# Kernel optimization log

Measured on AMD Instinct MI355X. Metric: run time of the kernel, lower is better.

The kernel has to match this reference:

```python
import jax, jax.numpy as jnp
import numpy as np

N_NODES = 50000
NEG_SLOPE = 0.2

def _segment_softmax(e, seg, n):
    m = jax.ops.segment_max(e, seg, num_segments=n)
    ex = jnp.exp(e - m[seg])
    s = jax.ops.segment_sum(ex, seg, num_segments=n)
    return ex / s[seg]

def _gatv2_layer(x, src, dst, n, Wl, bl, Wr, br, att):
    # GATv2 (heads=1): e_ij = att . leaky_relu(Wl x_j + Wr x_i); msg = alpha * Wl x_j
    xl = x @ Wl + bl            # [N, D] source transform
    xr = x @ Wr + br            # [N, D] target transform
    h = jax.nn.leaky_relu(xl[src] + xr[dst], NEG_SLOPE)  # [E, D]
    e = h @ att                 # [E]
    alpha = _segment_softmax(e, dst, n)
    out = jax.ops.segment_sum(alpha[:, None] * xl[src], dst, num_segments=n)
    return out

def setup_inputs() -> dict:
    key = jax.random.key(0)
    ks = jax.random.split(key, 16)
    N, E, Q, F, D, H = N_NODES, 800000, 200000, 128, 250, 256
    def glorot(k, shape):
        fan = shape[0] + shape[-1]
        return jax.random.uniform(k, shape, jnp.float32, -1.0, 1.0) * np.sqrt(6.0 / fan)
    return {
        "x": jax.random.normal(ks[0], (N, F), jnp.float32),
        "edge_index": jax.random.randint(ks[1], (2, E), 0, N, jnp.int32),
        "query": jax.random.randint(ks[2], (Q, 2), 0, N, jnp.int32),
        "W1l": glorot(ks[3], (F, D)), "b1l": jnp.zeros((D,), jnp.float32),
        "W1r": glorot(ks[4], (F, D)), "b1r": jnp.zeros((D,), jnp.float32),
        "att1": glorot(ks[5], (D,)),
        "W2l": glorot(ks[6], (D, D)), "b2l": jnp.zeros((D,), jnp.float32),
        "W2r": glorot(ks[7], (D, D)), "b2r": jnp.zeros((D,), jnp.float32),
        "att2": glorot(ks[8], (D,)),
        "Wm1": glorot(ks[9], (2 * D, H)), "bm1": jnp.zeros((H,), jnp.float32),
        "Wm2": glorot(ks[10], (H, 1)), "bm2": jnp.zeros((1,), jnp.float32),
    }

def reference(x, edge_index, query, W1l, b1l, W1r, b1r, att1,
              W2l, b2l, W2r, b2r, att2, Wm1, bm1, Wm2, bm2):
    n = x.shape[0]
    # add self loops (PyG default add_self_loops=True)
    loops = jnp.arange(n, dtype=edge_index.dtype)
    src = jnp.concatenate([edge_index[0], loops])
    dst = jnp.concatenate([edge_index[1], loops])
    h = _gatv2_layer(x, src, dst, n, W1l, b1l, W1r, b1r, att1)
    h = jax.nn.relu(h)
    emb = _gatv2_layer(h, src, dst, n, W2l, b2l, W2r, b2r, att2)
    # edge-prediction head: gather pair embeddings, concat, MLP
    pair = jnp.concatenate([emb[query[:, 0]], emb[query[:, 1]]], axis=1)  # [Q, 2D]
    out = jax.nn.relu(pair @ Wm1 + bm1)
    out = jax.nn.relu(out @ Wm2 + bm2)
    return out
```

## Files before the change

kernel.cpp:

```cpp
#include <hip/hip_runtime.h>
#include <hip/hip_fp16.h>
#include <math.h>
#include <stdint.h>

#define NN 50000
#define NE 800000
#define ET (NE + NN)
#define FIN 128
#define DD 250
#define HD 256
#define NQ 200000
#define NEG_SLOPE 0.2f

typedef unsigned short u16;
typedef __attribute__((ext_vector_type(4))) float f32x4;
typedef _Float16 h2v __attribute__((ext_vector_type(2)));
typedef _Float16 f16x8 __attribute__((ext_vector_type(8)));

union H2U { h2v h; unsigned int u; };

__device__ __forceinline__ u16 f2h(float v) {
    __half h = __float2half(v);
    return *reinterpret_cast<u16*>(&h);
}
__device__ __forceinline__ float4 ld4h(const u16* p) {
    uint2 r = *(const uint2*)p;
    __half2 a = *(__half2*)&r.x;
    __half2 b = *(__half2*)&r.y;
    float2 fa = __half22float2(a), fb = __half22float2(b);
    return make_float4(fa.x, fa.y, fb.x, fb.y);
}
__device__ __forceinline__ h2v hmax2v(h2v a, h2v b) {
    return __builtin_elementwise_max(a, b);
}


#define DPPMOV(v, ctrl, rm) \
    ((unsigned int)__builtin_amdgcn_update_dpp(0, (int)(v), (ctrl), (rm), 0xF, true))

__device__ __forceinline__ unsigned int h2_wave_sum63(h2v x) {
    H2U u, t; u.h = x;
    t.u = DPPMOV(u.u, 0x111, 0xF); u.h = u.h + t.h;
    t.u = DPPMOV(u.u, 0x112, 0xF); u.h = u.h + t.h;
    t.u = DPPMOV(u.u, 0x114, 0xF); u.h = u.h + t.h;
    t.u = DPPMOV(u.u, 0x118, 0xF); u.h = u.h + t.h;
    t.u = DPPMOV(u.u, 0x142, 0xA); u.h = u.h + t.h;
    t.u = DPPMOV(u.u, 0x143, 0xC); u.h = u.h + t.h;
    return (unsigned int)__builtin_amdgcn_readlane((int)u.u, 63);
}

__device__ __forceinline__ float f32_wave_sum63(float x) {
    union FU { float f; unsigned int u; } a, t, o;
    a.f = x;
    t.u = DPPMOV(a.u, 0x111, 0xF); a.f += t.f;
    t.u = DPPMOV(a.u, 0x112, 0xF); a.f += t.f;
    t.u = DPPMOV(a.u, 0x114, 0xF); a.f += t.f;
    t.u = DPPMOV(a.u, 0x118, 0xF); a.f += t.f;
    t.u = DPPMOV(a.u, 0x142, 0xA); a.f += t.f;
    t.u = DPPMOV(a.u, 0x143, 0xC); a.f += t.f;
    o.u = (unsigned int)__builtin_amdgcn_readlane((int)a.u, 63);
    return o.f;
}


__global__ __launch_bounds__(256) void scan1_kernel(
    int* __restrict__ cnt, int* __restrict__ rowptr, int* __restrict__ bsum)
{
    __shared__ int buf[256];
    int t = threadIdx.x;
    int i = blockIdx.x * 256 + t;
    int v = (i < NN) ? cnt[i] : 0;
    if (i < NN) cnt[i] = 0;
    buf[t] = v;
    __syncthreads();
#pragma unroll
    for (int off = 1; off < 256; off <<= 1) {
        int add = (t >= off) ? buf[t - off] : 0;
        __syncthreads();
        buf[t] += add;
        __syncthreads();
    }
    if (i < NN) rowptr[i] = buf[t] - v;
    if (t == 255) bsum[blockIdx.x] = buf[255];
}

__global__ __launch_bounds__(256) void scan2_kernel(
    int* __restrict__ bsum, int* __restrict__ rowptr, int nb)
{
    __shared__ int buf[256];
    int t = threadIdx.x;
    int v = (t < nb) ? bsum[t] : 0;
    buf[t] = v;
    __syncthreads();
#pragma unroll
    for (int off = 1; off < 256; off <<= 1) {
        int add = (t >= off) ? buf[t - off] : 0;
        __syncthreads();
        buf[t] += add;
        __syncthreads();
    }
    if (t < nb) bsum[t] = buf[t] - v;
    if (t == 255) rowptr[NN] = buf[255];
}

__global__ __launch_bounds__(256) void scan3_kernel(
    int* __restrict__ rowptr, const int* __restrict__ bsum)
{
    int i = blockIdx.x * 256 + threadIdx.x;
    if (i < NN) rowptr[i] += bsum[blockIdx.x];
}

__global__ void scatter_kernel(const int* __restrict__ ei,
                               const int* __restrict__ rowptr,
                               int* __restrict__ fill,
                               int* __restrict__ ssrc) {
    int k = blockIdx.x * 256 + threadIdx.x;
    if (k >= ET) return;
    int s, d;
    if (k < NE) { s = ei[k]; d = ei[NE + k]; }
    else        { s = k - NE; d = k - NE; }
    int pos = rowptr[d] + atomicAdd(&fill[d], 1);
    ssrc[pos] = s << 9;
}


#define CONVX_BLOCKS 3125

__global__ __launch_bounds__(256) void conv_all(
    const float* __restrict__ x, const int* __restrict__ ei,
    u16* __restrict__ Asp,
    const float* __restrict__ W1l, const float* __restrict__ W1r,
    const float* __restrict__ W2l, const float* __restrict__ W2r,
    const float* __restrict__ Wm1,
    const float* __restrict__ att1, const float* __restrict__ att2,
    u16* __restrict__ W1lT, u16* __restrict__ W1rT,
    u16* __restrict__ W2lT, u16* __restrict__ W2rT,
    u16* __restrict__ WmtT, u16* __restrict__ WmbT,
    u16* __restrict__ atth1, u16* __restrict__ atth2,
    int* __restrict__ cnt)
{
    if (blockIdx.x < CONVX_BLOCKS) {
        int tid = blockIdx.x * 256 + threadIdx.x;
        size_t idx = (size_t)tid * 8;
        if (idx >= (size_t)NN * FIN) return;
        float4 v0 = *(const float4*)(x + idx);
        float4 v1 = *(const float4*)(x + idx + 4);
        ushort4 o0, o1;
        o0.x = f2h(v0.x); o0.y = f2h(v0.y); o0.z = f2h(v0.z); o0.w = f2h(v0.w);
        o1.x = f2h(v1.x); o1.y = f2h(v1.y); o1.z = f2h(v1.z); o1.w = f2h(v1.w);
        *(ushort4*)(Asp + idx) = o0;
        *(ushort4*)(Asp + idx + 4) = o1;
        return;
    }
    int b = blockIdx.x - CONVX_BLOCKS;
    if (b < 1280) {
        const float* W; int K, N, koff, kshift, b0; u16* ot;
        if (b < 128)       { W = W1l; K = FIN; N = DD; koff = 0;  kshift = 7; b0 = 0;    ot = W1lT; }
        else if (b < 256)  { W = W1r; K = FIN; N = DD; koff = 0;  kshift = 7; b0 = 128;  ot = W1rT; }
        else if (b < 512)  { W = W2l; K = DD;  N = DD; koff = 0;  kshift = 8; b0 = 256;  ot = W2lT; }
        else if (b < 768)  { W = W2r; K = DD;  N = DD; koff = 0;  kshift = 8; b0 = 512;  ot = W2rT; }
        else if (b < 1024) { W = Wm1; K = DD;  N = HD; koff = 0;  kshift = 8; b0 = 768;  ot = WmtT; }
        else               { W = Wm1; K = DD;  N = HD; koff = DD; kshift = 8; b0 = 1024; ot = WmbT; }
        int id = (b - b0) * 256 + threadIdx.x;
        int Kp = 1 << kshift;
        int n = id >> kshift, k = id & (Kp - 1);
        float v = (n < N && k < K) ? W[(size_t)(k + koff) * N + n] : 0.f;
        ot[id] = f2h(v);
        return;
    }
    if (b < 1282) {
        const float* a = (b == 1280) ? att1 : att2;
        u16* o = (b == 1280) ? atth1 : atth2;
        int id = threadIdx.x;
        o[id] = f2h(id < DD ? a[id] : 0.f);
        return;
    }
    int k = (b - 1282) * 256 + threadIdx.x;
    if (k >= ET) return;
    int d = (k < NE) ? ei[NE + k] : (k - NE);
    atomicAdd(&cnt[d], 1);
}


#define AP 40

__global__ __launch_bounds__(512) void gemm_pair(
    const u16* __restrict__ A, int Kp,
    const u16* __restrict__ B0, const u16* __restrict__ B1,
    const float* __restrict__ bias0, const float* __restrict__ bias1,
    void* __restrict__ C0v, void* __restrict__ C1v, int M, int N, int fmt)
{
    __shared__ u16 AS[128][AP], B0S[256][AP], B1S[256][AP];

    int row0 = blockIdx.x * 128;
    int t = threadIdx.x;
    int lane = t & 63, w = t >> 6;
    int wr = w >> 2, wc = w & 3;
    int quad = lane >> 4, rr = lane & 15;

    f32x4 acc0[4][4], acc1[4][4];
#pragma unroll
    for (int i = 0; i < 4; i++)
#pragma unroll
        for (int j = 0; j < 4; j++) {
            acc0[i][j] = (f32x4){0.f, 0.f, 0.f, 0.f};
            acc1[i][j] = (f32x4){0.f, 0.f, 0.f, 0.f};
        }

    int arow = t >> 2, akc = (t & 3) * 8;
    bool aok = (row0 + arow) < M;
    const u16* pA   = A  + (size_t)(row0 + arow) * Kp + akc;
    int brow = t >> 2, bkc = akc;
    const u16* pB0a = B0 + (size_t)brow * Kp + bkc;
    const u16* pB0b = pB0a + (size_t)128 * Kp;
    const u16* pB1a = B1 + (size_t)brow * Kp + bkc;
    const u16* pB1b = pB1a + (size_t)128 * Kp;

    for (int k0 = 0; k0 < Kp; k0 += 32) {
        f16x8 a{};
        if (aok) a = *(const f16x8*)(pA + k0);
        *(f16x8*)&AS[arow][akc]            = a;
        *(f16x8*)&B0S[brow][bkc]           = *(const f16x8*)(pB0a + k0);
        *(f16x8*)&B0S[brow + 128][bkc]     = *(const f16x8*)(pB0b + k0);
        *(f16x8*)&B1S[brow][bkc]           = *(const f16x8*)(pB1a + k0);
        *(f16x8*)&B1S[brow + 128][bkc]     = *(const f16x8*)(pB1b + k0);
        __syncthreads();

        f16x8 fA[4];
#pragma unroll
        for (int fi = 0; fi < 4; fi++) {
            int r = wr * 64 + fi * 16 + rr;
            fA[fi] = *(const f16x8*)&AS[r][quad * 8];
        }
#pragma unroll
        for (int fj = 0; fj < 4; fj++) {
            int c = wc * 64 + fj * 16 + rr;
            f16x8 b0 = *(const f16x8*)&B0S[c][quad * 8];
            f16x8 b1 = *(const f16x8*)&B1S[c][quad * 8];
#pragma unroll
            for (int fi = 0; fi < 4; fi++) {
                acc0[fi][fj] = __builtin_amdgcn_mfma_f32_16x16x32_f16(fA[fi], b0, acc0[fi][fj], 0, 0, 0);
                acc1[fi][fj] = __builtin_amdgcn_mfma_f32_16x16x32_f16(fA[fi], b1, acc1[fi][fj], 0, 0, 0);
            }
        }
        __syncthreads();
    }

#pragma unroll
    for (int fj = 0; fj < 4; fj++) {
        int gc = wc * 64 + fj * 16 + rr;
        if (gc >= N) continue;
        float bb0 = bias0 ? bias0[gc] : 0.f;
        float bb1 = bias1 ? bias1[gc] : 0.f;
#pragma unroll
        for (int fi = 0; fi < 4; fi++) {
#pragma unroll
            for (int r = 0; r < 4; r++) {
                int grr = row0 + wr * 64 + fi * 16 + quad * 4 + r;
                if (grr < M) {
                    float v0 = acc0[fi][fj][r] + bb0;
                    float v1 = acc1[fi][fj][r] + bb1;
                    if (fmt & 1) ((u16*)C0v)[(size_t)grr * 256 + gc] = f2h(v0);
                    else         ((float*)C0v)[(size_t)grr * N + gc] = v0;
                    if (fmt & 2) ((u16*)C1v)[(size_t)grr * 256 + gc] = f2h(v1);
                    else         ((float*)C1v)[(size_t)grr * N + gc] = v1;
                }
            }
        }
    }
}


__global__ __launch_bounds__(256) void fused_edge_kernel(
    const int* __restrict__ rowptr, const int* __restrict__ ssrc,
    const u16* __restrict__ xl16, const u16* __restrict__ xr16,
    const u16* __restrict__ atth,
    u16* __restrict__ Oh, int dorelu)
{
    int i = blockIdx.x * 4 + (threadIdx.x >> 6);
    if (i >= NN) return;
    int lane = threadIdx.x & 63;
    int d0 = lane * 4;
    int lb = d0 * 2;

    uint2 atr = *(const uint2*)&atth[d0];
    h2v at0h = *(h2v*)&atr.x, at1h = *(h2v*)&atr.y;
    const h2v c02 = {(_Float16)0.2f, (_Float16)0.2f};
    const char* xlb = (const char*)xl16;

    uint2 xrr = *(const uint2*)&xr16[(size_t)i * 256 + d0];
    h2v xr0h = *(h2v*)&xrr.x, xr1h = *(h2v*)&xrr.y;

    int beg = __builtin_amdgcn_readfirstlane(rowptr[i]);
    int end = __builtin_amdgcn_readfirstlane(rowptr[i + 1]);

    float m = -1e30f, ssum = 0.f;
    float4 acc = make_float4(0.f, 0.f, 0.f, 0.f);

    auto ldrow = [&](int o) -> uint2 {
        return *(const uint2*)(xlb + o + lb);
    };
    auto edge_score = [&](uint2 g) -> float {
        h2v x0 = *(h2v*)&g.x, x1 = *(h2v*)&g.y;
        h2v s = x0 + xr0h; s = hmax2v(s, s * c02);
        float e = __builtin_amdgcn_fdot2(s, at0h, 0.f, false);
        s = x1 + xr1h; s = hmax2v(s, s * c02);
        return __builtin_amdgcn_fdot2(s, at1h, e, false);
    };
    auto single_update = [&](uint2 g) {
        float e = f32_wave_sum63(edge_score(g));
        h2v x0 = *(h2v*)&g.x, x1 = *(h2v*)&g.y;
        float nm = fmaxf(m, e);
        float sc = __expf(m - nm);
        float w = __expf(e - nm);
        acc.x = fmaf(w, (float)x0.x, acc.x * sc);
        acc.y = fmaf(w, (float)x0.y, acc.y * sc);
        acc.z = fmaf(w, (float)x1.x, acc.z * sc);
        acc.w = fmaf(w, (float)x1.y, acc.w * sc);
        ssum = fmaf(ssum, sc, w);
        m = nm;
    };

    int p = beg;
    if (p + 3 < end) {
        int o0 = __builtin_amdgcn_readfirstlane(ssrc[p]);
        int o1 = __builtin_amdgcn_readfirstlane(ssrc[p + 1]);
        int o2 = __builtin_amdgcn_readfirstlane(ssrc[p + 2]);
        int o3 = __builtin_amdgcn_readfirstlane(ssrc[p + 3]);
        uint2 a0 = ldrow(o0), a1 = ldrow(o1), a2 = ldrow(o2), a3 = ldrow(o3);

        bool hB = (p + 7 < end);
        uint2 b0, b1, b2, b3;
        if (hB) {
            int q0 = __builtin_amdgcn_readfirstlane(ssrc[p + 4]);
            int q1 = __builtin_amdgcn_readfirstlane(ssrc[p + 5]);
            int q2 = __builtin_amdgcn_readfirstlane(ssrc[p + 6]);
            int q3 = __builtin_amdgcn_readfirstlane(ssrc[p + 7]);
            b0 = ldrow(q0); b1 = ldrow(q1); b2 = ldrow(q2); b3 = ldrow(q3);
        }
        bool hC = (p + 11 < end);
        int co0 = 0, co1 = 0, co2 = 0, co3 = 0;
        if (hC) {
            co0 = __builtin_amdgcn_readfirstlane(ssrc[p + 8]);
            co1 = __builtin_amdgcn_readfirstlane(ssrc[p + 9]);
            co2 = __builtin_amdgcn_readfirstlane(ssrc[p + 10]);
            co3 = __builtin_amdgcn_readfirstlane(ssrc[p + 11]);
        }

        for (;;) {
            uint2 cg0, cg1, cg2, cg3;
            if (hC) {
                cg0 = ldrow(co0); cg1 = ldrow(co1); cg2 = ldrow(co2); cg3 = ldrow(co3);
            }
            bool hD = (p + 15 < end);
            int do0 = 0, do1 = 0, do2 = 0, do3 = 0;
            if (hD) {
                do0 = __builtin_amdgcn_readfirstlane(ssrc[p + 12]);
                do1 = __builtin_amdgcn_readfirstlane(ssrc[p + 13]);
                do2 = __builtin_amdgcn_readfirstlane(ssrc[p + 14]);
                do3 = __builtin_amdgcn_readfirstlane(ssrc[p + 15]);
            }

            h2v x00 = *(h2v*)&a0.x, x01 = *(h2v*)&a0.y;
            h2v x10 = *(h2v*)&a1.x, x11 = *(h2v*)&a1.y;
            h2v x20 = *(h2v*)&a2.x, x21 = *(h2v*)&a2.y;
            h2v x30 = *(h2v*)&a3.x, x31 = *(h2v*)&a3.y;

            h2v s;
            float e0, e1, e2, e3;
            s = x00 + xr0h; s = hmax2v(s, s * c02);
            e0 = __builtin_amdgcn_fdot2(s, at0h, 0.f, false);
            s = x01 + xr1h; s = hmax2v(s, s * c02);
            e0 = __builtin_amdgcn_fdot2(s, at1h, e0, false);
            s = x10 + xr0h; s = hmax2v(s, s * c02);
            e1 = __builtin_amdgcn_fdot2(s, at0h, 0.f, false);
            s = x11 + xr1h; s = hmax2v(s, s * c02);
            e1 = __builtin_amdgcn_fdot2(s, at1h, e1, false);
            s = x20 + xr0h; s = hmax2v(s, s * c02);
            e2 = __builtin_amdgcn_fdot2(s, at0h, 0.f, false);
            s = x21 + xr1h; s = hmax2v(s, s * c02);
            e2 = __builtin_amdgcn_fdot2(s, at1h, e2, false);
            s = x30 + xr0h; s = hmax2v(s, s * c02);
            e3 = __builtin_amdgcn_fdot2(s, at0h, 0.f, false);
            s = x31 + xr1h; s = hmax2v(s, s * c02);
            e3 = __builtin_amdgcn_fdot2(s, at1h, e3, false);

            H2U u01, u23, r01, r23;
            u01.h.x = (_Float16)e0; u01.h.y = (_Float16)e1;
            u23.h.x = (_Float16)e2; u23.h.y = (_Float16)e3;
            r01.u = h2_wave_sum63(u01.h);
            r23.u = h2_wave_sum63(u23.h);
            float es0 = (float)r01.h.x, es1 = (float)r01.h.y;
            float es2 = (float)r23.h.x, es3 = (float)r23.h.y;

            float nm = fmaxf(fmaxf(m, es0), fmaxf(fmaxf(es1, es2), es3));
            float sc = __expf(m - nm);
            float w0 = __expf(es0 - nm);
            float w1 = __expf(es1 - nm);
            float w2 = __expf(es2 - nm);
            float w3 = __expf(es3 - nm);
            float ax0 = fmaf(w1, (float)x10.x, w0 * (float)x00.x);
            float ax1 = fmaf(w3, (float)x30.x, w2 * (float)x20.x);
            float ay0 = fmaf(w1, (float)x10.y, w0 * (float)x00.y);
            float ay1 = fmaf(w3, (float)x30.y, w2 * (float)x20.y);
            float az0 = fmaf(w1, (float)x11.x, w0 * (float)x01.x);
            float az1 = fmaf(w3, (float)x31.x, w2 * (float)x21.x);
            float aw0 = fmaf(w1, (float)x11.y, w0 * (float)x01.y);
            float aw1 = fmaf(w3, (float)x31.y, w2 * (float)x21.y);
            acc.x = fmaf(acc.x, sc, ax0 + ax1);
            acc.y = fmaf(acc.y, sc, ay0 + ay1);
            acc.z = fmaf(acc.z, sc, az0 + az1);
            acc.w = fmaf(acc.w, sc, aw0 + aw1);
            ssum = fmaf(ssum, sc, (w0 + w1) + (w2 + w3));
            m = nm;

            p += 4;
            if (!hB) break;
            a0 = b0; a1 = b1; a2 = b2; a3 = b3;
            b0 = cg0; b1 = cg1; b2 = cg2; b3 = cg3;
            hB = hC; hC = hD;
            co0 = do0; co1 = do1; co2 = do2; co3 = do3;
        }
    }

    int rem = end - p;
    if (rem > 0) {
        int o0 = __builtin_amdgcn_readfirstlane(ssrc[p]);
        int o1 = 0, o2 = 0;
        if (rem > 1) o1 = __builtin_amdgcn_readfirstlane(ssrc[p + 1]);
        if (rem > 2) o2 = __builtin_amdgcn_readfirstlane(ssrc[p + 2]);
        uint2 g0 = ldrow(o0);
        uint2 g1, g2;
        if (rem > 1) g1 = ldrow(o1);
        if (rem > 2) g2 = ldrow(o2);
        single_update(g0);
        if (rem > 1) single_update(g1);
        if (rem > 2) single_update(g2);
    }

    float inv = 1.f / ssum;
    acc.x *= inv; acc.y *= inv; acc.z *= inv; acc.w *= inv;
    if (dorelu) {
        acc.x = fmaxf(acc.x, 0.f); acc.y = fmaxf(acc.y, 0.f);
        acc.z = fmaxf(acc.z, 0.f); acc.w = fmaxf(acc.w, 0.f);
    }
    size_t obase = (size_t)i * 256 + d0;
    ushort4 hv;
    hv.x = f2h(acc.x); hv.y = f2h(acc.y); hv.z = f2h(acc.z); hv.w = f2h(acc.w);
    *(ushort4*)&Oh[obase] = hv;
}


__global__ __launch_bounds__(256) void query_kernel(
    const int* __restrict__ qry, const u16* __restrict__ Ptop,
    const u16* __restrict__ Pbot, const float* __restrict__ Wm2,
    const float* __restrict__ bm2, float* __restrict__ out)
{
    int q = (blockIdx.x * 4 + (threadIdx.x >> 6)) * 2;
    if (q >= NQ) return;
    int lane = threadIdx.x & 63;
    int a0 = __builtin_amdgcn_readfirstlane(qry[q * 2 + 0]);
    int b0 = __builtin_amdgcn_readfirstlane(qry[q * 2 + 1]);
    int a1 = __builtin_amdgcn_readfirstlane(qry[q * 2 + 2]);
    int b1 = __builtin_amdgcn_readfirstlane(qry[q * 2 + 3]);
    float4 w  = *(const float4*)&Wm2[lane * 4];
    float4 t0 = ld4h(&Ptop[(size_t)a0 * HD + lane * 4]);
    float4 v0 = ld4h(&Pbot[(size_t)b0 * HD + lane * 4]);
    float4 t1 = ld4h(&Ptop[(size_t)a1 * HD + lane * 4]);
    float4 v1 = ld4h(&Pbot[(size_t)b1 * HD + lane * 4]);
    float s0 = fmaxf(t0.x + v0.x, 0.f) * w.x + fmaxf(t0.y + v0.y, 0.f) * w.y
             + fmaxf(t0.z + v0.z, 0.f) * w.z + fmaxf(t0.w + v0.w, 0.f) * w.w;
    float s1 = fmaxf(t1.x + v1.x, 0.f) * w.x + fmaxf(t1.y + v1.y, 0.f) * w.y
             + fmaxf(t1.z + v1.z, 0.f) * w.z + fmaxf(t1.w + v1.w, 0.f) * w.w;
    s0 = f32_wave_sum63(s0);
    s1 = f32_wave_sum63(s1);
    if (lane == 0) {
        float bb = bm2[0];
        out[q] = fmaxf(s0 + bb, 0.f);
        if (q + 1 < NQ) out[q + 1] = fmaxf(s1 + bb, 0.f);
    }
}


extern "C" void kernel_launch(void* const* d_in, const int* in_sizes, int n_in,
                              void* d_out, int out_size, void* d_ws, size_t ws_size,
                              hipStream_t stream) {
    const float* x    = (const float*)d_in[0];
    const int*   ei   = (const int*)d_in[1];
    const int*   qry  = (const int*)d_in[2];
    const float* W1l  = (const float*)d_in[3];
    const float* b1l  = (const float*)d_in[4];
    const float* W1r  = (const float*)d_in[5];
    const float* b1r  = (const float*)d_in[6];
    const float* att1 = (const float*)d_in[7];
    const float* W2l  = (const float*)d_in[8];
    const float* b2l  = (const float*)d_in[9];
    const float* W2r  = (const float*)d_in[10];
    const float* b2r  = (const float*)d_in[11];
    const float* att2 = (const float*)d_in[12];
    const float* Wm1  = (const float*)d_in[13];
    const float* bm1  = (const float*)d_in[14];
    const float* Wm2  = (const float*)d_in[15];
    const float* bm2  = (const float*)d_in[16];
    float* out = (float*)d_out;

    u16* xl16    = (u16*)d_ws;
    u16* xr16    = xl16 + (size_t)NN * 256;
    int* rowptr  = (int*)(xr16 + (size_t)NN * 256);
    int* fill    = rowptr + NN + 1;
    int* ssrc    = fill + NN;
    int* bsum    = ssrc + ET;
    u16* atth1   = (u16*)(bsum + 256);
    u16* atth2   = atth1 + 256;
    uintptr_t wp = (uintptr_t)(atth2 + 256);
    wp = (wp + 63) & ~(uintptr_t)63;
    u16* W1lT = (u16*)wp;
    u16* W1rT = W1lT + 256 * 128;
    u16* W2lT = W1rT + 256 * 128;
    u16* W2rT = W2lT + 65536;
    u16* WmtT = W2rT + 65536;
    u16* WmbT = WmtT + 65536;
    u16* Asp  = WmbT + 65536;
    u16* Ptop16 = xl16;
    u16* Pbot16 = xr16;

    dim3 blk(256);
    int gET = (ET + 255) / 256;
    int gNode = (NN + 3) / 4;
    int nb = (NN + 255) / 256;
    int gg = (NN + 127) / 128;

    hipMemsetAsync(fill, 0, (size_t)NN * sizeof(int), stream);
    conv_all<<<CONVX_BLOCKS + 1282 + gET, blk, 0, stream>>>(x, ei, Asp,
        W1l, W1r, W2l, W2r, Wm1, att1, att2,
        W1lT, W1rT, W2lT, W2rT, WmtT, WmbT, atth1, atth2, fill);

    scan1_kernel<<<nb, blk, 0, stream>>>(fill, rowptr, bsum);
    scan2_kernel<<<1, blk, 0, stream>>>(bsum, rowptr, nb);
    scan3_kernel<<<nb, blk, 0, stream>>>(rowptr, bsum);
    scatter_kernel<<<gET, blk, 0, stream>>>(ei, rowptr, fill, ssrc);

    gemm_pair<<<gg, dim3(512), 0, stream>>>(Asp, 128, W1lT, W1rT,
                                      b1l, b1r, (void*)xl16, (void*)xr16, NN, DD, 3);
    fused_edge_kernel<<<gNode, blk, 0, stream>>>(rowptr, ssrc, xl16, xr16, atth1, Asp, 1);

    gemm_pair<<<gg, dim3(512), 0, stream>>>(Asp, 256, W2lT, W2rT,
                                      b2l, b2r, (void*)xl16, (void*)xr16, NN, DD, 3);
    fused_edge_kernel<<<gNode, blk, 0, stream>>>(rowptr, ssrc, xl16, xr16, atth2, Asp, 0);

    gemm_pair<<<gg, dim3(512), 0, stream>>>(Asp, 256, WmtT, WmbT,
                                      bm1, (const float*)nullptr, (void*)Ptop16, (void*)Pbot16, NN, HD, 3);

    query_kernel<<<(NQ / 2 + 3) / 4, blk, 0, stream>>>(qry, Ptop16, Pbot16, Wm2, bm2, out);
}
```

Baseline: 511.8 us.

## Double-buffer GEMM LDS tiles with XOR swizzle and batch four queries per wave

The pair GEMM now keeps two LDS stages. It prefetches the next K-slice into registers while MFMAs run on the current slice, so only one barrier is needed per iteration. The LDS layout changes from a padded row of 40 to an XOR-swizzled row of 32 to avoid bank conflicts. The query kernel handles four queries per wave instead of two, which halves the number of blocks and adds memory-level parallelism. In exchange, the GEMM uses more registers and LDS, which may reduce occupancy.

```diff
diff --git a/kernel.cpp b/kernel.cpp
--- a/kernel.cpp
+++ b/kernel.cpp
@@ -182,21 +182,20 @@
 }
 
 
-#define AP 40
-
 __global__ __launch_bounds__(512) void gemm_pair(
     const u16* __restrict__ A, int Kp,
     const u16* __restrict__ B0, const u16* __restrict__ B1,
     const float* __restrict__ bias0, const float* __restrict__ bias1,
     void* __restrict__ C0v, void* __restrict__ C1v, int M, int N, int fmt)
 {
-    __shared__ u16 AS[128][AP], B0S[256][AP], B1S[256][AP];
+    __shared__ u16 AS[2][128][32], B0S[2][256][32], B1S[2][256][32];
 
     int row0 = blockIdx.x * 128;
     int t = threadIdx.x;
     int lane = t & 63, w = t >> 6;
     int wr = w >> 2, wc = w & 3;
     int quad = lane >> 4, rr = lane & 15;
+    int rcol = (quad ^ ((rr >> 1) & 3)) * 8;
 
     f32x4 acc0[4][4], acc1[4][4];
 #pragma unroll
@@ -207,43 +206,71 @@
             acc1[i][j] = (f32x4){0.f, 0.f, 0.f, 0.f};
         }
 
-    int arow = t >> 2, akc = (t & 3) * 8;
-    bool aok = (row0 + arow) < M;
-    const u16* pA   = A  + (size_t)(row0 + arow) * Kp + akc;
-    int brow = t >> 2, bkc = akc;
-    const u16* pB0a = B0 + (size_t)brow * Kp + bkc;
+    int sr = t >> 2, sg = t & 3;
+    int scol = (sg ^ ((sr >> 1) & 3)) * 8;
+    bool aok = (row0 + sr) < M;
+    const u16* pA   = A  + (size_t)(row0 + sr) * Kp + sg * 8;
+    const u16* pB0a = B0 + (size_t)sr * Kp + sg * 8;
     const u16* pB0b = pB0a + (size_t)128 * Kp;
-    const u16* pB1a = B1 + (size_t)brow * Kp + bkc;
+    const u16* pB1a = B1 + (size_t)sr * Kp + sg * 8;
     const u16* pB1b = pB1a + (size_t)128 * Kp;
 
+    {
+        f16x8 ra{};
+        if (aok) ra = *(const f16x8*)pA;
+        f16x8 rb0a = *(const f16x8*)pB0a;
+        f16x8 rb0b = *(const f16x8*)pB0b;
+        f16x8 rb1a = *(const f16x8*)pB1a;
+        f16x8 rb1b = *(const f16x8*)pB1b;
+        *(f16x8*)&AS[0][sr][scol]        = ra;
+        *(f16x8*)&B0S[0][sr][scol]       = rb0a;
+        *(f16x8*)&B0S[0][sr + 128][scol] = rb0b;
+        *(f16x8*)&B1S[0][sr][scol]       = rb1a;
+        *(f16x8*)&B1S[0][sr + 128][scol] = rb1b;
+    }
+    __syncthreads();
+
+    int cur = 0;
     for (int k0 = 0; k0 < Kp; k0 += 32) {
-        f16x8 a{};
-        if (aok) a = *(const f16x8*)(pA + k0);
-        *(f16x8*)&AS[arow][akc]            = a;
-        *(f16x8*)&B0S[brow][bkc]           = *(const f16x8*)(pB0a + k0);
-        *(f16x8*)&B0S[brow + 128][bkc]     = *(const f16x8*)(pB0b + k0);
-        *(f16x8*)&B1S[brow][bkc]           = *(const f16x8*)(pB1a + k0);
-        *(f16x8*)&B1S[brow + 128][bkc]     = *(const f16x8*)(pB1b + k0);
-        __syncthreads();
+        int kn = k0 + 32;
+        bool more = kn < Kp;
+        f16x8 ra{}, rb0a{}, rb0b{}, rb1a{}, rb1b{};
+        if (more) {
+            if (aok) ra = *(const f16x8*)(pA + kn);
+            rb0a = *(const f16x8*)(pB0a + kn);
+            rb0b = *(const f16x8*)(pB0b + kn);
+            rb1a = *(const f16x8*)(pB1a + kn);
+            rb1b = *(const f16x8*)(pB1b + kn);
+        }
 
         f16x8 fA[4];
 #pragma unroll
         for (int fi = 0; fi < 4; fi++) {
             int r = wr * 64 + fi * 16 + rr;
-            fA[fi] = *(const f16x8*)&AS[r][quad * 8];
+            fA[fi] = *(const f16x8*)&AS[cur][r][rcol];
         }
 #pragma unroll
         for (int fj = 0; fj < 4; fj++) {
             int c = wc * 64 + fj * 16 + rr;
-            f16x8 b0 = *(const f16x8*)&B0S[c][quad * 8];
-            f16x8 b1 = *(const f16x8*)&B1S[c][quad * 8];
+            f16x8 b0 = *(const f16x8*)&B0S[cur][c][rcol];
+            f16x8 b1 = *(const f16x8*)&B1S[cur][c][rcol];
 #pragma unroll
             for (int fi = 0; fi < 4; fi++) {
                 acc0[fi][fj] = __builtin_amdgcn_mfma_f32_16x16x32_f16(fA[fi], b0, acc0[fi][fj], 0, 0, 0);
                 acc1[fi][fj] = __builtin_amdgcn_mfma_f32_16x16x32_f16(fA[fi], b1, acc1[fi][fj], 0, 0, 0);
             }
         }
-        __syncthreads();
+
+        if (more) {
+            int nb_ = cur ^ 1;
+            *(f16x8*)&AS[nb_][sr][scol]        = ra;
+            *(f16x8*)&B0S[nb_][sr][scol]       = rb0a;
+            *(f16x8*)&B0S[nb_][sr + 128][scol] = rb0b;
+            *(f16x8*)&B1S[nb_][sr][scol]       = rb1a;
+            *(f16x8*)&B1S[nb_][sr + 128][scol] = rb1b;
+            __syncthreads();
+            cur = nb_;
+        }
     }
 
 #pragma unroll
@@ -456,28 +483,44 @@
     const u16* __restrict__ Pbot, const float* __restrict__ Wm2,
     const float* __restrict__ bm2, float* __restrict__ out)
 {
-    int q = (blockIdx.x * 4 + (threadIdx.x >> 6)) * 2;
+    int q = (blockIdx.x * 4 + (threadIdx.x >> 6)) * 4;
     if (q >= NQ) return;
     int lane = threadIdx.x & 63;
     int a0 = __builtin_amdgcn_readfirstlane(qry[q * 2 + 0]);
     int b0 = __builtin_amdgcn_readfirstlane(qry[q * 2 + 1]);
     int a1 = __builtin_amdgcn_readfirstlane(qry[q * 2 + 2]);
     int b1 = __builtin_amdgcn_readfirstlane(qry[q * 2 + 3]);
+    int a2 = __builtin_amdgcn_readfirstlane(qry[q * 2 + 4]);
+    int b2 = __builtin_amdgcn_readfirstlane(qry[q * 2 + 5]);
+    int a3 = __builtin_amdgcn_readfirstlane(qry[q * 2 + 6]);
+    int b3 = __builtin_amdgcn_readfirstlane(qry[q * 2 + 7]);
     float4 w  = *(const float4*)&Wm2[lane * 4];
     float4 t0 = ld4h(&Ptop[(size_t)a0 * HD + lane * 4]);
     float4 v0 = ld4h(&Pbot[(size_t)b0 * HD + lane * 4]);
     float4 t1 = ld4h(&Ptop[(size_t)a1 * HD + lane * 4]);
     float4 v1 = ld4h(&Pbot[(size_t)b1 * HD + lane * 4]);
+    float4 t2 = ld4h(&Ptop[(size_t)a2 * HD + lane * 4]);
+    float4 v2 = ld4h(&Pbot[(size_t)b2 * HD + lane * 4]);
+    float4 t3 = ld4h(&Ptop[(size_t)a3 * HD + lane * 4]);
+    float4 v3 = ld4h(&Pbot[(size_t)b3 * HD + lane * 4]);
     float s0 = fmaxf(t0.x + v0.x, 0.f) * w.x + fmaxf(t0.y + v0.y, 0.f) * w.y
              + fmaxf(t0.z + v0.z, 0.f) * w.z + fmaxf(t0.w + v0.w, 0.f) * w.w;
     float s1 = fmaxf(t1.x + v1.x, 0.f) * w.x + fmaxf(t1.y + v1.y, 0.f) * w.y
              + fmaxf(t1.z + v1.z, 0.f) * w.z + fmaxf(t1.w + v1.w, 0.f) * w.w;
+    float s2 = fmaxf(t2.x + v2.x, 0.f) * w.x + fmaxf(t2.y + v2.y, 0.f) * w.y
+             + fmaxf(t2.z + v2.z, 0.f) * w.z + fmaxf(t2.w + v2.w, 0.f) * w.w;
+    float s3 = fmaxf(t3.x + v3.x, 0.f) * w.x + fmaxf(t3.y + v3.y, 0.f) * w.y
+             + fmaxf(t3.z + v3.z, 0.f) * w.z + fmaxf(t3.w + v3.w, 0.f) * w.w;
     s0 = f32_wave_sum63(s0);
     s1 = f32_wave_sum63(s1);
+    s2 = f32_wave_sum63(s2);
+    s3 = f32_wave_sum63(s3);
     if (lane == 0) {
         float bb = bm2[0];
-        out[q] = fmaxf(s0 + bb, 0.f);
-        if (q + 1 < NQ) out[q + 1] = fmaxf(s1 + bb, 0.f);
+        out[q]     = fmaxf(s0 + bb, 0.f);
+        out[q + 1] = fmaxf(s1 + bb, 0.f);
+        out[q + 2] = fmaxf(s2 + bb, 0.f);
+        out[q + 3] = fmaxf(s3 + bb, 0.f);
     }
 }
 
@@ -551,5 +594,5 @@
     gemm_pair<<<gg, dim3(512), 0, stream>>>(Asp, 256, WmtT, WmbT,
                                       bm1, (const float*)nullptr, (void*)Ptop16, (void*)Pbot16, NN, HD, 3);
 
-    query_kernel<<<(NQ / 2 + 3) / 4, blk, 0, stream>>>(qry, Ptop16, Pbot16, Wm2, bm2, out);
-}
+    query_kernel<<<(NQ / 4 + 3) / 4, blk, 0, stream>>>(qry, Ptop16, Pbot16, Wm2, bm2, out);
+}
```

Result: faster. 488.6 us (-4.5%).
